# Optimization experiments

Hardware: AMD Instinct MI355X
Metric: run time of the kernel (lower is better)

Reference implementation:

```python
import jax, jax.numpy as jnp
import numpy as np


def _sig_gram(X, Y, n):
    """Signature-kernel gram matrix via the Goursat PDE recurrence.
    X: (A, M, D), Y: (B, N, D). Returns (A, B) of k(x_a, y_b).
    Recurrence: K[i+1,j+1] = K[i+1,j] + K[i,j+1] + K[i,j]*(inc_ij - 1).
    """
    f = 2 ** n
    # dyadic refinement: increments scaled by 1/2^n, each repeated 2^n times
    dX = jnp.repeat((X[:, 1:] - X[:, :-1]) / f, f, axis=1)  # (A, Mg-1, D)
    dY = jnp.repeat((Y[:, 1:] - Y[:, :-1]) / f, f, axis=1)  # (B, Ng-1, D)
    inc = jnp.einsum('aid,bjd->abij', dX, dY)               # (A, B, Mg-1, Ng-1)
    A, B, _, Ng1 = inc.shape
    ones_col = jnp.ones((A, B, 1), inc.dtype)

    def row_step(K_prev, inc_row):
        # K_prev: row i of the PDE grid, shape (A,B,Ng1+1); inc_row: (A,B,Ng1)
        diag = K_prev[..., :-1] * (inc_row - 1.0)  # K[i,j]*inc - K[i,j]
        up = K_prev[..., 1:]                        # K[i,j+1]

        def col_step(k_left, uv):
            u, d = uv
            k = k_left + u + d
            return k, k

        _, krow = jax.lax.scan(
            col_step,
            jnp.ones((A, B), inc.dtype),
            (jnp.moveaxis(up, -1, 0), jnp.moveaxis(diag, -1, 0)),
        )
        K_new = jnp.concatenate([ones_col, jnp.moveaxis(krow, 0, -1)], axis=-1)
        return K_new, None

    K0 = jnp.ones((A, B, Ng1 + 1), inc.dtype)  # boundary row K[0,:] = 1
    K_last, _ = jax.lax.scan(row_step, K0, jnp.moveaxis(inc, 2, 0))
    return K_last[..., -1]  # K[-1,-1] for every pair


def setup_inputs() -> dict:
    key = jax.random.key(0)
    kx, ky = jax.random.split(key)
    SCALE = 0.05  # keep kernel values in fp32 range (exponential growth)
    X = jax.random.normal(kx, (64, 128, 16), dtype=jnp.float32) * SCALE
    Y = jax.random.normal(ky, (64, 128, 16), dtype=jnp.float32) * SCALE
    return {"X": X, "Y": Y, "n": 0}


def reference(X, Y, n):
    k_xx = _sig_gram(X, X, n)
    k_yy = _sig_gram(Y, Y, n)
    k_xy = _sig_gram(X, Y, n)
    return jnp.mean(k_xx) + jnp.mean(k_yy) - 2.0 * jnp.mean(k_xy)
```

## Files before the change

### kernel.cpp

```cpp
#include <hip/hip_runtime.h>


#define XY_BLOCKS 1024
#define TRI_BLOCKS 544
#define NBLOCKS (XY_BLOCKS + 2 * TRI_BLOCKS)
#define DINC_PER 130048
#define WS_OUT_OFF (2 * DINC_PER)
#define NOUT (NBLOCKS * 4)

template <int C, int RM, int BM, bool BC>
__device__ __forceinline__ float dpp0(float x) {
    return __builtin_bit_cast(float, __builtin_amdgcn_update_dpp(
        0, __builtin_bit_cast(int, x), C, RM, BM, BC));
}

__device__ __forceinline__ float wave_scan_incl(float v) {
    v += dpp0<0x111, 0xf, 0xf, true>(v);
    v += dpp0<0x112, 0xf, 0xf, true>(v);
    v += dpp0<0x114, 0xf, 0xf, true>(v);
    v += dpp0<0x118, 0xf, 0xf, true>(v);
    v += dpp0<0x142, 0xa, 0xf, false>(v);
    v += dpp0<0x143, 0xc, 0xf, false>(v);
    return v;
}

__device__ __forceinline__ float wave_shr1(float x, float oldv) {
    return __builtin_bit_cast(float, __builtin_amdgcn_update_dpp(
        __builtin_bit_cast(int, oldv), __builtin_bit_cast(int, x),
        0x138, 0xf, 0xf, false));
}

__global__ __launch_bounds__(256) void sig_diff(
    const float* __restrict__ X, const float* __restrict__ Y,
    float* __restrict__ dInc)
{
    int i = blockIdx.x * 256 + threadIdx.x;
    if (i >= 65024) return;
    int which = (i >= 32512) ? 1 : 0;
    int j = i - which * 32512;
    int a = j / 508;
    int rq = j - a * 508;
    const float* S = which ? Y : X;
    const float4* p = (const float4*)(S + a * 2048) + rq;
    float4 v0 = p[0], v1 = p[4];
    float4 d;
    d.x = v1.x - v0.x; d.y = v1.y - v0.y;
    d.z = v1.z - v0.z; d.w = v1.w - v0.w;
    ((float4*)dInc)[i] = d;
}

__global__ __launch_bounds__(256) void sig_pde2(
    const float* __restrict__ dInc, float* __restrict__ outw)
{
    const int B = blockIdx.x;
    const int w = threadIdx.x >> 6, lane = threadIdx.x & 63;

    int g, a, b0;
    if (B < XY_BLOCKS) {
        g = 2; a = B >> 4; b0 = (B & 15) << 2;
    } else {
        int t = B - XY_BLOCKS; g = 0;
        if (t >= TRI_BLOCKS) { t -= TRI_BLOCKS; g = 1; }
        int aa = 0;
        for (;;) { int nb = (67 - aa) >> 2; if (t < nb) break; t -= nb; ++aa; }
        a = aa; b0 = aa + (t << 2);
    }
    const int b = b0 + w;
    const int slot = (B << 2) + w;
    if (g < 2 && b > 63) { if (lane == 0) outw[slot] = 0.0f; return; }

    const float* dXb = dInc;
    const float* dYb = dInc + DINC_PER;
    const float* dA = (g == 1) ? dYb : dXb;
    const float* dB = (g == 0) ? dXb : dYb;
    const float weight = (g == 2) ? (-2.0f / 4096.0f)
                                  : ((a == b ? 1.0f : 2.0f) / 4096.0f);

    float ya[16], yb_[16];
    {
        const float* Qb = dB + b * 2032;
        const int j0 = lane << 1;
        const int j1 = (j0 + 1 < 127) ? j0 + 1 : 126;
        const float4* A4 = (const float4*)(Qb + j0 * 16);
        const float4* B4 = (const float4*)(Qb + j1 * 16);
#pragma unroll
        for (int q = 0; q < 4; ++q) {
            float4 va = A4[q], vb = B4[q];
            ya[4*q+0] = va.x; ya[4*q+1] = va.y; ya[4*q+2] = va.z; ya[4*q+3] = va.w;
            yb_[4*q+0] = vb.x; yb_[4*q+1] = vb.y; yb_[4*q+2] = vb.z; yb_[4*q+3] = vb.w;
        }
    }

    const int abase = __builtin_amdgcn_readfirstlane(a * 2032);
    const float4* Ar = (const float4*)(dA + abase);

    float xr[16], xn[16];
#pragma unroll
    for (int q = 0; q < 4; ++q) {
        float4 v = Ar[q];
        xr[4*q+0] = v.x; xr[4*q+1] = v.y; xr[4*q+2] = v.z; xr[4*q+3] = v.w;
    }

    float g_lo = 1.0f, g_hi = 1.0f;
    const bool last = (lane == 63);

    for (int r = 0; r < 127; ++r) {
        const int rn = (r < 126) ? r + 1 : 126;
#pragma unroll
        for (int q = 0; q < 4; ++q) {
            float4 v = Ar[4 * rn + q];
            xn[4*q+0] = v.x; xn[4*q+1] = v.y; xn[4*q+2] = v.z; xn[4*q+3] = v.w;
        }
        float s0 = -0.5f, s1 = -0.5f, t0 = -0.5f, t1 = -0.5f;
#pragma unroll
        for (int d = 0; d < 16; d += 2) {
            s0 = fmaf(xr[d], ya[d], s0);    s1 = fmaf(xr[d+1], ya[d+1], s1);
            t0 = fmaf(xr[d], yb_[d], t0);   t1 = fmaf(xr[d+1], yb_[d+1], t1);
        }
        const float i0 = s0 + s1;
        const float i1 = t0 + t1;

        const float gl = wave_shr1(g_hi, 1.0f);
        const float c0 = fmaf(gl, i0, g_lo);
        const float c1 = last ? 0.0f : fmaf(g_lo, i1, g_hi);
        const float S = wave_scan_incl(c0 + c1);
        g_lo = (S - c1) + 1.0f;
        g_hi = S + 1.0f;
#pragma unroll
        for (int d = 0; d < 16; ++d) xr[d] = xn[d];
    }

    const float kab = __builtin_bit_cast(float,
        __builtin_amdgcn_readlane(__builtin_bit_cast(int, g_lo), 63));
    if (lane == 0) outw[slot] = weight * kab;
}

__global__ __launch_bounds__(256) void sig_reduce2(
    const float* __restrict__ v, float* __restrict__ out, int n)
{
    __shared__ float red[256];
    float s = 0.0f;
    for (int i = threadIdx.x; i < n; i += 256) s += v[i];
    red[threadIdx.x] = s;
    __syncthreads();
    for (int st = 128; st > 0; st >>= 1) {
        if (threadIdx.x < st) red[threadIdx.x] += red[threadIdx.x + st];
        __syncthreads();
    }
    if (threadIdx.x == 0) out[0] = red[0];
}

__global__ __launch_bounds__(64) void sig_pde_kernel(
    const float* __restrict__ X, const float* __restrict__ Y,
    float* __restrict__ ws)
{
    __shared__ float Xs[2048];
    const int T = blockIdx.x;
    const int g = T >> 12;
    const int t = T & 4095;
    const int a = t >> 6, b = t & 63;
    const int lane = threadIdx.x;
    if (g < 2 && a > b) { if (lane == 0) ws[T] = 0.0f; return; }
    const float* P = (g == 1) ? Y : X;
    const float* Q = (g == 0) ? X : Y;
    const float weight = (g == 2) ? (-2.0f / 4096.0f)
                                  : ((a == b ? 1.0f : 2.0f) / 4096.0f);
    {
        const float4* Pa = (const float4*)(P + a * 2048);
        float4* Xs4 = (float4*)Xs;
#pragma unroll
        for (int k = 0; k < 8; ++k) Xs4[lane + (k << 6)] = Pa[lane + (k << 6)];
    }
    __syncthreads();
    {
        float tmp[32];
#pragma unroll
        for (int k = 0; k < 32; ++k) {
            int idx = lane + (k << 6);
            tmp[k] = (idx < 2032) ? (Xs[idx + 16] - Xs[idx]) : 0.0f;
        }
        __syncthreads();
#pragma unroll
        for (int k = 0; k < 32; ++k) {
            int idx = lane + (k << 6);
            if (idx < 2032) Xs[idx] = tmp[k];
        }
    }
    __syncthreads();
    float y0[16], y1[16];
    {
        const float* Qb = Q + b * 2048;
        const int r0 = lane << 1;
        const int r2 = (r0 + 2 > 127) ? 127 : (r0 + 2);
        const float4* A4 = (const float4*)(Qb + r0 * 16);
        const float4* B4 = (const float4*)(Qb + (r0 + 1) * 16);
        const float4* C4 = (const float4*)(Qb + r2 * 16);
#pragma unroll
        for (int q = 0; q < 4; ++q) {
            float4 ra = A4[q], rb = B4[q], rc = C4[q];
            y0[4*q+0] = rb.x - ra.x;  y1[4*q+0] = rc.x - rb.x;
            y0[4*q+1] = rb.y - ra.y;  y1[4*q+1] = rc.y - rb.y;
            y0[4*q+2] = rb.z - ra.z;  y1[4*q+2] = rc.z - rb.z;
            y0[4*q+3] = rb.w - ra.w;  y1[4*q+3] = rc.w - rb.w;
        }
    }
    float g_lo = 1.0f, g_hi = 1.0f;
    const bool last = (lane == 63);
    for (int r = 0; r < 127; ++r) {
        const float* xrow = Xs + r * 16;
        float s0 = -0.5f, s1 = -0.5f, t0 = -0.5f, t1 = -0.5f;
#pragma unroll
        for (int d = 0; d < 16; d += 2) {
            s0 = fmaf(xrow[d], y0[d], s0);   s1 = fmaf(xrow[d+1], y0[d+1], s1);
            t0 = fmaf(xrow[d], y1[d], t0);   t1 = fmaf(xrow[d+1], y1[d+1], t1);
        }
        const float i0 = s0 + s1, i1 = t0 + t1;
        const float gl = wave_shr1(g_hi, 1.0f);
        const float c0 = fmaf(gl, i0, g_lo);
        const float c1 = last ? 0.0f : fmaf(g_lo, i1, g_hi);
        const float S = wave_scan_incl(c0 + c1);
        g_lo = (S - c1) + 1.0f;
        g_hi = S + 1.0f;
    }
    const float kab = __builtin_bit_cast(float,
        __builtin_amdgcn_readlane(__builtin_bit_cast(int, g_lo), 63));
    if (lane == 0) ws[T] = weight * kab;
}

extern "C" void kernel_launch(void* const* d_in, const int* in_sizes, int n_in,
                              void* d_out, int out_size, void* d_ws, size_t ws_size,
                              hipStream_t stream) {
    const float* X = (const float*)d_in[0];
    const float* Y = (const float*)d_in[1];
    float* out = (float*)d_out;
    float* ws  = (float*)d_ws;

    const size_t need = (size_t)(WS_OUT_OFF + NOUT) * sizeof(float);
    if (ws_size >= need) {
        sig_diff<<<254, 256, 0, stream>>>(X, Y, ws);
        sig_pde2<<<NBLOCKS, 256, 0, stream>>>(ws, ws + WS_OUT_OFF);
        sig_reduce2<<<1, 256, 0, stream>>>(ws + WS_OUT_OFF, out, NOUT);
    } else {
        sig_pde_kernel<<<12288, 64, 0, stream>>>(X, Y, ws);
        sig_reduce2<<<1, 256, 0, stream>>>(ws, out, 12288);
    }
}
```

Before: 147.1 us.

## Rebalance PDE work across waves and fuse final reduction via atomics

Replaces the block-of-four-pairs mapping, which left idle waves in triangle blocks, with a flat task list of 8256 pairs spread over 8192 waves. Every 129th wave takes one extra pair. The separate reduction kernel is removed: each block sums its weighted results and atomically adds them to the output, which the diff kernel zeroes first. The row loop is unrolled by two to avoid register copies. The cost is some load imbalance from the waves that run two pairs, and a nondeterministic floating-point summation order.

```diff
diff --git a/kernel.cpp b/kernel.cpp
--- a/kernel.cpp
+++ b/kernel.cpp
@@ -1,12 +1,10 @@
 #include <hip/hip_runtime.h>
 
 
-#define XY_BLOCKS 1024
-#define TRI_BLOCKS 544
-#define NBLOCKS (XY_BLOCKS + 2 * TRI_BLOCKS)
 #define DINC_PER 130048
-#define WS_OUT_OFF (2 * DINC_PER)
-#define NOUT (NBLOCKS * 4)
+#define NWAVES 8192
+#define NTASK 8256
+#define NBLOCKS3 2048
 
 template <int C, int RM, int BM, bool BC>
 __device__ __forceinline__ float dpp0(float x) {
@@ -32,8 +30,9 @@
 
 __global__ __launch_bounds__(256) void sig_diff(
     const float* __restrict__ X, const float* __restrict__ Y,
-    float* __restrict__ dInc)
-{
+    float* __restrict__ dInc, float* __restrict__ out)
+{
+    if (blockIdx.x == 0 && threadIdx.x == 0) out[0] = 0.0f;
     int i = blockIdx.x * 256 + threadIdx.x;
     if (i >= 65024) return;
     int which = (i >= 32512) ? 1 : 0;
@@ -49,90 +48,116 @@
     ((float4*)dInc)[i] = d;
 }
 
-__global__ __launch_bounds__(256) void sig_pde2(
-    const float* __restrict__ dInc, float* __restrict__ outw)
-{
-    const int B = blockIdx.x;
-    const int w = threadIdx.x >> 6, lane = threadIdx.x & 63;
-
-    int g, a, b0;
-    if (B < XY_BLOCKS) {
-        g = 2; a = B >> 4; b0 = (B & 15) << 2;
-    } else {
-        int t = B - XY_BLOCKS; g = 0;
-        if (t >= TRI_BLOCKS) { t -= TRI_BLOCKS; g = 1; }
-        int aa = 0;
-        for (;;) { int nb = (67 - aa) >> 2; if (t < nb) break; t -= nb; ++aa; }
-        a = aa; b0 = aa + (t << 2);
-    }
-    const int b = b0 + w;
-    const int slot = (B << 2) + w;
-    if (g < 2 && b > 63) { if (lane == 0) outw[slot] = 0.0f; return; }
-
-    const float* dXb = dInc;
-    const float* dYb = dInc + DINC_PER;
-    const float* dA = (g == 1) ? dYb : dXb;
-    const float* dB = (g == 0) ? dXb : dYb;
-    const float weight = (g == 2) ? (-2.0f / 4096.0f)
-                                  : ((a == b ? 1.0f : 2.0f) / 4096.0f);
-
-    float ya[16], yb_[16];
-    {
-        const float* Qb = dB + b * 2032;
-        const int j0 = lane << 1;
-        const int j1 = (j0 + 1 < 127) ? j0 + 1 : 126;
-        const float4* A4 = (const float4*)(Qb + j0 * 16);
-        const float4* B4 = (const float4*)(Qb + j1 * 16);
+__global__ __launch_bounds__(256, 8) void sig_pde3(
+    const float* __restrict__ dInc, float* __restrict__ out)
+{
+    __shared__ float red[4];
+    const int wid  = threadIdx.x >> 6;
+    const int lane = threadIdx.x & 63;
+    const int gw   = (blockIdx.x << 2) + wid;
+
+    float acc = 0.0f;
+    const int nextra = ((gw % 129) == 0) ? 1 : 0;
+
+#pragma unroll 1
+    for (int it = 0; it <= nextra; ++it) {
+        const int t = it ? (NWAVES + gw / 129) : gw;
+
+        int g, a, b;
+        if (t < 4096) {
+            g = 2; a = t >> 6; b = t & 63;
+        } else {
+            int tt = t - 4096;
+            g = 0;
+            if (tt >= 2080) { g = 1; tt -= 2080; }
+            int aa = 0;
+            for (;;) { int nb = 64 - aa; if (tt < nb) break; tt -= nb; ++aa; }
+            a = aa; b = aa + tt;
+        }
+
+        const float* dA = (g == 1) ? (dInc + DINC_PER) : dInc;
+        const float* dB = (g == 0) ? dInc : (dInc + DINC_PER);
+        const float weight = (g == 2) ? (-2.0f / 4096.0f)
+                                      : ((a == b ? 1.0f : 2.0f) / 4096.0f);
+
+        float ya[16], yb_[16];
+        {
+            const float* Qb = dB + b * 2032;
+            const int j0 = lane << 1;
+            const int j1 = (j0 + 1 < 127) ? j0 + 1 : 126;
+            const float4* A4 = (const float4*)(Qb + j0 * 16);
+            const float4* B4 = (const float4*)(Qb + j1 * 16);
+#pragma unroll
+            for (int q = 0; q < 4; ++q) {
+                float4 va = A4[q], vb = B4[q];
+                ya[4*q+0]=va.x;  ya[4*q+1]=va.y;  ya[4*q+2]=va.z;  ya[4*q+3]=va.w;
+                yb_[4*q+0]=vb.x; yb_[4*q+1]=vb.y; yb_[4*q+2]=vb.z; yb_[4*q+3]=vb.w;
+            }
+        }
+#pragma unroll
+        for (int d = 0; d < 16; ++d)
+            asm volatile("" : "+v"(ya[d]), "+v"(yb_[d]));
+
+        const int abase = __builtin_amdgcn_readfirstlane(a * 2032);
+        const float4* Ar = (const float4*)(dA + abase);
+
+        float xr[16], xn[16];
 #pragma unroll
         for (int q = 0; q < 4; ++q) {
-            float4 va = A4[q], vb = B4[q];
-            ya[4*q+0] = va.x; ya[4*q+1] = va.y; ya[4*q+2] = va.z; ya[4*q+3] = va.w;
-            yb_[4*q+0] = vb.x; yb_[4*q+1] = vb.y; yb_[4*q+2] = vb.z; yb_[4*q+3] = vb.w;
-        }
-    }
-
-    const int abase = __builtin_amdgcn_readfirstlane(a * 2032);
-    const float4* Ar = (const float4*)(dA + abase);
-
-    float xr[16], xn[16];
-#pragma unroll
-    for (int q = 0; q < 4; ++q) {
-        float4 v = Ar[q];
-        xr[4*q+0] = v.x; xr[4*q+1] = v.y; xr[4*q+2] = v.z; xr[4*q+3] = v.w;
-    }
-
-    float g_lo = 1.0f, g_hi = 1.0f;
-    const bool last = (lane == 63);
-
-    for (int r = 0; r < 127; ++r) {
-        const int rn = (r < 126) ? r + 1 : 126;
-#pragma unroll
-        for (int q = 0; q < 4; ++q) {
-            float4 v = Ar[4 * rn + q];
-            xn[4*q+0] = v.x; xn[4*q+1] = v.y; xn[4*q+2] = v.z; xn[4*q+3] = v.w;
-        }
-        float s0 = -0.5f, s1 = -0.5f, t0 = -0.5f, t1 = -0.5f;
-#pragma unroll
-        for (int d = 0; d < 16; d += 2) {
-            s0 = fmaf(xr[d], ya[d], s0);    s1 = fmaf(xr[d+1], ya[d+1], s1);
-            t0 = fmaf(xr[d], yb_[d], t0);   t1 = fmaf(xr[d+1], yb_[d+1], t1);
-        }
-        const float i0 = s0 + s1;
-        const float i1 = t0 + t1;
-
-        const float gl = wave_shr1(g_hi, 1.0f);
-        const float c0 = fmaf(gl, i0, g_lo);
-        const float c1 = last ? 0.0f : fmaf(g_lo, i1, g_hi);
-        const float S = wave_scan_incl(c0 + c1);
-        g_lo = (S - c1) + 1.0f;
-        g_hi = S + 1.0f;
-#pragma unroll
-        for (int d = 0; d < 16; ++d) xr[d] = xn[d];
-    }
-
-    const float kab = __builtin_bit_cast(float,
-        __builtin_amdgcn_readlane(__builtin_bit_cast(int, g_lo), 63));
-    if (lane == 0) outw[slot] = weight * kab;
+            float4 v = Ar[q];
+            xr[4*q+0]=v.x; xr[4*q+1]=v.y; xr[4*q+2]=v.z; xr[4*q+3]=v.w;
+        }
+
+        float g_lo = 1.0f, g_hi = 1.0f;
+        const bool last = (lane == 63);
+
+#define SIG_ROW(XROW)                                                       \
+        {                                                                   \
+            float s0=-0.5f, s1=-0.5f, t0=-0.5f, t1=-0.5f;                   \
+            _Pragma("unroll")                                               \
+            for (int d = 0; d < 16; d += 2) {                               \
+                s0 = fmaf(XROW[d],   ya[d],    s0);                         \
+                s1 = fmaf(XROW[d+1], ya[d+1],  s1);                         \
+                t0 = fmaf(XROW[d],   yb_[d],   t0);                         \
+                t1 = fmaf(XROW[d+1], yb_[d+1], t1);                         \
+            }                                                               \
+            const float i0 = s0 + s1;                 \
+            const float i1 = t0 + t1;                 \
+            const float gl = wave_shr1(g_hi, 1.0f);           \
+            const float c0 = fmaf(gl, i0, g_lo);                            \
+            const float c1 = last ? 0.0f : fmaf(g_lo, i1, g_hi);            \
+            const float S  = wave_scan_incl(c0 + c1);                       \
+            g_lo = (S - c1) + 1.0f;                                         \
+            g_hi = S + 1.0f;                                                \
+        }
+
+#pragma unroll 1
+        for (int r = 0; r < 126; r += 2) {
+#pragma unroll
+            for (int q = 0; q < 4; ++q) {
+                float4 v = Ar[4*(r+1)+q];
+                xn[4*q+0]=v.x; xn[4*q+1]=v.y; xn[4*q+2]=v.z; xn[4*q+3]=v.w;
+            }
+            SIG_ROW(xr)
+#pragma unroll
+            for (int q = 0; q < 4; ++q) {
+                float4 v = Ar[4*(r+2)+q];
+                xr[4*q+0]=v.x; xr[4*q+1]=v.y; xr[4*q+2]=v.z; xr[4*q+3]=v.w;
+            }
+            SIG_ROW(xn)
+        }
+        SIG_ROW(xr)
+#undef SIG_ROW
+
+        const float kab = __builtin_bit_cast(float,
+            __builtin_amdgcn_readlane(__builtin_bit_cast(int, g_lo), 63));
+        acc = fmaf(weight, kab, acc);
+    }
+
+    if (lane == 0) red[wid] = acc;
+    __syncthreads();
+    if (threadIdx.x == 0)
+        atomicAdd(out, (red[0] + red[1]) + (red[2] + red[3]));
 }
 
 __global__ __launch_bounds__(256) void sig_reduce2(
@@ -235,11 +260,10 @@
     float* out = (float*)d_out;
     float* ws  = (float*)d_ws;
 
-    const size_t need = (size_t)(WS_OUT_OFF + NOUT) * sizeof(float);
+    const size_t need = (size_t)(2 * DINC_PER) * sizeof(float);
     if (ws_size >= need) {
-        sig_diff<<<254, 256, 0, stream>>>(X, Y, ws);
-        sig_pde2<<<NBLOCKS, 256, 0, stream>>>(ws, ws + WS_OUT_OFF);
-        sig_reduce2<<<1, 256, 0, stream>>>(ws + WS_OUT_OFF, out, NOUT);
+        sig_diff<<<254, 256, 0, stream>>>(X, Y, ws, out);
+        sig_pde3<<<NBLOCKS3, 256, 0, stream>>>(ws, out);
     } else {
         sig_pde_kernel<<<12288, 64, 0, stream>>>(X, Y, ws);
         sig_reduce2<<<1, 256, 0, stream>>>(ws, out, 12288);
```

After: 205.0 us. 39.4% more time.
